# Kernel tuning notes

Measured on AMD Instinct MI355X. Metric: run time of the kernel, lower is better.

## Reference

```python
import jax, jax.numpy as jnp
import numpy as np

B, T, D, H, L = 32, 512, 256, 512, 3


def setup_inputs() -> dict:
    key = jax.random.key(0)
    ks = jax.random.split(key, 14)
    def lin(k, fan_in, shape):
        return jax.random.normal(k, shape, jnp.float32) / np.sqrt(fan_in)
    inp = {"x": jax.random.normal(ks[0], (B, T, D), jnp.float32)}
    dims_in = [D, H, H]
    i = 1
    for l in range(L):
        inp[f"Wi{l}"] = lin(ks[i + 0], dims_in[l], (3 * H, dims_in[l]))
        inp[f"bi{l}"] = lin(ks[i + 1], dims_in[l], (3 * H,))
        inp[f"Wh{l}"] = lin(ks[i + 2], H, (3 * H, H))
        inp[f"bh{l}"] = lin(ks[i + 3], H, (3 * H,))
        i += 4
    return inp


def _cell(Wi, bi, Wh, bh, xin, h):
    # faithful to ExponentialGatingGRUCell (h2h term appears twice in n preact)
    h2h = h @ Wh.T + bh                      # [B, 3H]
    preact = xin @ Wi.T + bi + h2h           # [B, 3H]
    g = jax.nn.sigmoid(preact[:, : 2 * H])
    r, z = g[:, :H], g[:, H:]
    r = jnp.exp(-jnp.exp(-r))
    z = jnp.exp(-jnp.exp(-z))
    n = jnp.tanh(preact[:, 2 * H:] + r * h2h[:, 2 * H:])
    return (1.0 - z) * n + z * h


def _forward(x, params):
    h0 = tuple(jnp.zeros((x.shape[0], H), x.dtype) for _ in range(L))

    def step(carry, x_t):
        hs = list(carry)
        inp = x_t
        for l in range(L):
            Wi, bi, Wh, bh = params[l]
            hs[l] = _cell(Wi, bi, Wh, bh, inp, hs[l])
            inp = hs[l]
        return tuple(hs), None

    hT, _ = jax.lax.scan(step, h0, jnp.swapaxes(x, 0, 1))  # scan over time
    return hT[-1][:, None, :]  # [B, 1, H]


def reference(x, Wi0, bi0, Wh0, bh0, Wi1, bi1, Wh1, bh1, Wi2, bi2, Wh2, bh2):
    params = [(Wi0, bi0, Wh0, bh0), (Wi1, bi1, Wh1, bh1), (Wi2, bi2, Wh2, bh2)]
    return _forward(x, params)
```

## Files before the change

kernel.cpp:

```cpp
#include <hip/hip_runtime.h>
#include <hip/hip_bf16.h>

typedef __attribute__((ext_vector_type(4))) float fx4;
typedef __attribute__((ext_vector_type(8))) short bf8;
typedef __attribute__((ext_vector_type(4))) short sx4;
typedef __attribute__((ext_vector_type(4))) int ix4;

#define NBLK 96
#define HSZ (32 * 512)

__device__ __forceinline__ short f2bf(float f) {
  __hip_bfloat16 h = __float2bfloat16(f);
  return *reinterpret_cast<short*>(&h);
}
__device__ __forceinline__ float bf2f(short s) {
  union { unsigned u; float f; } c; c.u = ((unsigned)(unsigned short)s) << 16; return c.f;
}
__device__ __forceinline__ float rcpf(float x) { return __builtin_amdgcn_rcpf(x); }
__device__ __forceinline__ bf8 asbf8(ix4 v) { union { ix4 i; bf8 b; } u; u.i = v; return u.b; }

#define LDH(dst, p, OFF) \
  asm volatile("global_load_dwordx4 %0, %1, off offset:" OFF " sc0 sc1" \
               : "=v"(dst) : "v"(p) : "memory")
#define LDP(dst, p, OFF) \
  asm volatile("global_load_dwordx4 %0, %1, off offset:" OFF \
               : "=v"(dst) : "v"(p) : "memory")

#define LDH8(A, P) do { \
  LDH(A[0], P, "0");   LDH(A[1], P, "64");  LDH(A[2], P, "128"); LDH(A[3], P, "192"); \
  LDH(A[4], P, "256"); LDH(A[5], P, "320"); LDH(A[6], P, "384"); LDH(A[7], P, "448"); } while (0)
#define LDP4(A, P) do { \
  LDP(A[0], P, "0");   LDP(A[1], P, "64");  LDP(A[2], P, "128"); LDP(A[3], P, "192"); } while (0)

__global__ __launch_bounds__(256) void conv_x_k(const float* __restrict__ x,
                                                short* __restrict__ xhi, short* __restrict__ xlo) {
  int i = blockIdx.x * 256 + threadIdx.x;
  fx4 v = *(const fx4*)(x + (size_t)i * 4);
  int k = (i * 4) & 255;
  int row = (i * 4) >> 8;
  int b = row >> 9, t = row & 511;
  sx4 hi, lo;
#pragma unroll
  for (int e = 0; e < 4; ++e) {
    hi[e] = f2bf(v[e]);
    lo[e] = f2bf(v[e] - bf2f(hi[e]));
  }
  size_t o = ((size_t)(t * 32 + b)) * 256 + k;
  *(sx4*)(xhi + o) = hi;
  *(sx4*)(xlo + o) = lo;
}

__global__ __launch_bounds__(256, 1) void rec3(
    const short* __restrict__ xth, const short* __restrict__ xtl,
    const float* __restrict__ Wi0, const float* __restrict__ bi0,
    const float* __restrict__ Wh0, const float* __restrict__ bh0,
    const float* __restrict__ Wi1, const float* __restrict__ bi1,
    const float* __restrict__ Wh1, const float* __restrict__ bh1,
    const float* __restrict__ Wi2, const float* __restrict__ bi2,
    const float* __restrict__ Wh2, const float* __restrict__ bh2,
    short* __restrict__ hg, int* flags, float* __restrict__ out)
{
  __shared__ __align__(16) float m_lds[4][32][52];
  __shared__ float bi_s[48], bh_s[48];
  const int tid = threadIdx.x;
  const int bid = blockIdx.x;
  const int l = bid >> 5, p = bid & 31, j0 = p * 16;
  const int w = tid >> 6, lane = tid & 63, lm = lane & 15, lk = lane >> 4;
  const bool inW = (w < 2);

  const float *Wi, *bi, *Wh, *bh;
  if (l == 0)      { Wi = Wi0; bi = bi0; Wh = Wh0; bh = bh0; }
  else if (l == 1) { Wi = Wi1; bi = bi1; Wh = Wh1; bh = bh1; }
  else             { Wi = Wi2; bi = bi2; Wh = Wh2; bh = bh2; }
  const int Kin = (l == 0) ? 256 : 512;
  const int ksn = inW ? (Kin >> 6) : 8;
  const int kbase = inW ? w * (Kin >> 1) : (w - 2) * 256;
  const float* Wf = inW ? Wi : Wh;
  const int wstride = inW ? Kin : 512;

  bf8 bwh[3][8], bwl[3][8];
#pragma unroll
  for (int g = 0; g < 3; ++g) {
    const int grow = g * 512 + j0 + lm;
#pragma unroll
    for (int ks = 0; ks < 8; ++ks) if (ks < ksn) {
      const float* src = Wf + (size_t)grow * wstride + kbase + ks * 32 + lk * 8;
      fx4 f0 = *(const fx4*)(src);
      fx4 f1 = *(const fx4*)(src + 4);
      bf8 vh, vl;
#pragma unroll
      for (int e = 0; e < 4; ++e) {
        vh[e] = f2bf(f0[e]);     vl[e] = f2bf(f0[e] - bf2f(vh[e]));
        vh[4 + e] = f2bf(f1[e]); vl[4 + e] = f2bf(f1[e] - bf2f(vh[4 + e]));
      }
      bwh[g][ks] = vh; bwl[g][ks] = vl;
    }
  }
  if (tid < 48) {
    bi_s[tid] = bi[(tid >> 4) * 512 + j0 + (tid & 15)];
    bh_s[tid] = bh[(tid >> 4) * 512 + j0 + (tid & 15)];
  }

  short* hgl = hg + (size_t)l * 4 * HSZ;
  const short* hgp = hg + (size_t)(l - 1) * 4 * HSZ;
  {
    const int b = tid >> 3, zc = (tid & 7) * 2;
    __hip_atomic_store((int*)(hgl + (size_t)2 * HSZ + b * 512 + j0 + zc), 0,
                       __ATOMIC_RELAXED, __HIP_MEMORY_SCOPE_AGENT);
    __hip_atomic_store((int*)(hgl + (size_t)3 * HSZ + b * 512 + j0 + zc), 0,
                       __ATOMIC_RELAXED, __HIP_MEMORY_SCOPE_AGENT);
  }
  __syncthreads();
  if (tid == 0)
    __hip_atomic_store(flags + bid * 32, 1, __ATOMIC_RELAXED, __HIP_MEMORY_SCOPE_AGENT);

  const int cb = tid >> 3, c2 = (tid & 7) * 2;
  float hv0 = 0.f, hv1 = 0.f;

  for (int t = 0; t < 514; ++t) {
    const int s = t - l;
    const bool active = ((unsigned)s < 512u);

    ix4 rh[2][8], rl[2][8];
    if (active && l == 0 && inW) {
      const short* x0h = xth + (size_t)(s * 32 + lm) * 256 + kbase + lk * 8;
      const short* x1h = x0h + 16 * 256;
      const short* x0l = xtl + (size_t)(s * 32 + lm) * 256 + kbase + lk * 8;
      const short* x1l = x0l + 16 * 256;
      LDP4(rh[0], x0h); LDP4(rh[1], x1h);
      LDP4(rl[0], x0l); LDP4(rl[1], x1l);
    }

    if (tid < NBLK) {
      while (__hip_atomic_load(flags + tid * 32, __ATOMIC_RELAXED,
                               __HIP_MEMORY_SCOPE_AGENT) < t + 1) {}
    }
    __syncthreads();

    if (active) {
      if (!(l == 0 && inW)) {
        const short* basep = inW ? (hgp + (size_t)((s & 1) * 2) * HSZ)
                                 : (hgl + (size_t)(((s - 1) & 1) * 2) * HSZ);
        const short* s0h = basep + (size_t)lm * 512 + kbase + lk * 8;
        const short* s1h = s0h + 16 * 512;
        const short* s0l = s0h + HSZ;
        const short* s1l = s1h + HSZ;
        LDH8(rh[0], s0h); LDH8(rh[1], s1h);
        LDH8(rl[0], s0l); LDH8(rl[1], s1l);
      }
      asm volatile("s_waitcnt vmcnt(0)" ::: "memory");
      __builtin_amdgcn_sched_barrier(0);

      fx4 acc[2][3];
#pragma unroll
      for (int mt = 0; mt < 2; ++mt)
#pragma unroll
        for (int g = 0; g < 3; ++g) acc[mt][g] = (fx4){0.f, 0.f, 0.f, 0.f};
#pragma unroll
      for (int ks = 0; ks < 8; ++ks) if (ks < ksn) {
#pragma unroll
        for (int mt = 0; mt < 2; ++mt) {
          bf8 ah = asbf8(rh[mt][ks]);
          bf8 al = asbf8(rl[mt][ks]);
#pragma unroll
          for (int g = 0; g < 3; ++g) {
            acc[mt][g] = __builtin_amdgcn_mfma_f32_16x16x32_bf16(ah, bwh[g][ks], acc[mt][g], 0, 0, 0);
            acc[mt][g] = __builtin_amdgcn_mfma_f32_16x16x32_bf16(al, bwh[g][ks], acc[mt][g], 0, 0, 0);
            acc[mt][g] = __builtin_amdgcn_mfma_f32_16x16x32_bf16(ah, bwl[g][ks], acc[mt][g], 0, 0, 0);
          }
        }
      }
#pragma unroll
      for (int mt = 0; mt < 2; ++mt)
#pragma unroll
        for (int g = 0; g < 3; ++g)
#pragma unroll
          for (int q = 0; q < 4; ++q)
            m_lds[w][mt * 16 + lk * 4 + q][g * 16 + lm] = acc[mt][g][q];
      __syncthreads();

      float av[3][2], hh[3][2];
#pragma unroll
      for (int g = 0; g < 3; ++g)
#pragma unroll
        for (int e = 0; e < 2; ++e) {
          const int c = g * 16 + c2 + e;
          av[g][e] = m_lds[0][cb][c] + m_lds[1][cb][c] + bi_s[c];
          hh[g][e] = m_lds[2][cb][c] + m_lds[3][cb][c] + bh_s[c];
        }
      float hvv[2] = {hv0, hv1}, hn[2];
#pragma unroll
      for (int e = 0; e < 2; ++e) {
        float pr = av[0][e] + hh[0][e];
        float pz = av[1][e] + hh[1][e];
        float h2n = hh[2][e];
        float pn = av[2][e] + h2n;
        float sr = rcpf(1.f + __expf(-pr));
        float rr = __expf(-__expf(-sr));
        float sz = rcpf(1.f + __expf(-pz));
        float zz = __expf(-__expf(-sz));
        float na = pn + rr * h2n;
        float ex = __expf(2.f * na);
        float nn = 1.f - 2.f * rcpf(ex + 1.f);
        hn[e] = (1.f - zz) * nn + zz * hvv[e];
      }
      hv0 = hn[0]; hv1 = hn[1];
      short h0h = f2bf(hn[0]), h0l = f2bf(hn[0] - bf2f(h0h));
      short h1h = f2bf(hn[1]), h1l = f2bf(hn[1] - bf2f(h1h));
      int packh = (int)(unsigned short)h0h | ((int)(unsigned short)h1h << 16);
      int packl = (int)(unsigned short)h0l | ((int)(unsigned short)h1l << 16);

      short* hw = hgl + (size_t)((s & 1) * 2) * HSZ;
      __hip_atomic_store((int*)(hw + (size_t)cb * 512 + j0 + c2), packh,
                         __ATOMIC_RELAXED, __HIP_MEMORY_SCOPE_AGENT);
      __hip_atomic_store((int*)(hw + HSZ + (size_t)cb * 512 + j0 + c2), packl,
                         __ATOMIC_RELAXED, __HIP_MEMORY_SCOPE_AGENT);
      if (l == 2 && s == 511) {
        out[(size_t)cb * 512 + j0 + c2] = hn[0];
        out[(size_t)cb * 512 + j0 + c2 + 1] = hn[1];
      }
      __syncthreads();
    }
    if (tid == 0)
      __hip_atomic_store(flags + bid * 32, t + 2,
                         __ATOMIC_RELAXED, __HIP_MEMORY_SCOPE_AGENT);
  }
}

extern "C" void kernel_launch(void* const* d_in, const int* in_sizes, int n_in,
                              void* d_out, int out_size, void* d_ws, size_t ws_size,
                              hipStream_t stream) {
  const float* x   = (const float*)d_in[0];
  const float* Wi0 = (const float*)d_in[1];
  const float* bi0 = (const float*)d_in[2];
  const float* Wh0 = (const float*)d_in[3];
  const float* bh0 = (const float*)d_in[4];
  const float* Wi1 = (const float*)d_in[5];
  const float* bi1 = (const float*)d_in[6];
  const float* Wh1 = (const float*)d_in[7];
  const float* bh1 = (const float*)d_in[8];
  const float* Wi2 = (const float*)d_in[9];
  const float* bi2 = (const float*)d_in[10];
  const float* Wh2 = (const float*)d_in[11];
  const float* bh2 = (const float*)d_in[12];
  float* out = (float*)d_out;
  (void)in_sizes; (void)n_in; (void)out_size; (void)ws_size;

  char* ws = (char*)d_ws;
  size_t off = 0;
  auto alloc = [&](size_t b) { char* p = ws + off; off = (off + b + 255) & ~(size_t)255; return p; };
  short* xth   = (short*)alloc(16384ull * 256 * 2);
  short* xtl   = (short*)alloc(16384ull * 256 * 2);
  short* hg    = (short*)alloc(3ull * 4 * HSZ * 2);
  int*   flags = (int*)alloc(NBLK * 32 * 4);

  hipMemsetAsync(flags, 0, NBLK * 32 * 4, stream);
  hipLaunchKernelGGL(conv_x_k, dim3(4096), dim3(256), 0, stream, x, xth, xtl);
  hipLaunchKernelGGL(rec3, dim3(NBLK), dim3(256), 0, stream,
                     xth, xtl,
                     Wi0, bi0, Wh0, bh0,
                     Wi1, bi1, Wh1, bh1,
                     Wi2, bi2, Wh2, bh2,
                     hg, flags, out);
}
```

Measured before the change: 3.340 ms.

## Replace global barrier with per-layer dependency flags and triple-buffered hidden state

Result: no change. 3.296 ms (-1.3%).

```diff
diff --git a/kernel.cpp b/kernel.cpp
--- a/kernel.cpp
+++ b/kernel.cpp
@@ -25,12 +25,9 @@
 #define LDP(dst, p, OFF) \
   asm volatile("global_load_dwordx4 %0, %1, off offset:" OFF \
                : "=v"(dst) : "v"(p) : "memory")
-
-#define LDH8(A, P) do { \
-  LDH(A[0], P, "0");   LDH(A[1], P, "64");  LDH(A[2], P, "128"); LDH(A[3], P, "192"); \
-  LDH(A[4], P, "256"); LDH(A[5], P, "320"); LDH(A[6], P, "384"); LDH(A[7], P, "448"); } while (0)
-#define LDP4(A, P) do { \
-  LDP(A[0], P, "0");   LDP(A[1], P, "64");  LDP(A[2], P, "128"); LDP(A[3], P, "192"); } while (0)
+#define LD8(OP, A, P) do { \
+  OP(A[0], P, "0");   OP(A[1], P, "64");  OP(A[2], P, "128"); OP(A[3], P, "192"); \
+  OP(A[4], P, "256"); OP(A[5], P, "320"); OP(A[6], P, "384"); OP(A[7], P, "448"); } while (0)
 
 __global__ __launch_bounds__(256) void conv_x_k(const float* __restrict__ x,
                                                 short* __restrict__ xhi, short* __restrict__ xlo) {
@@ -48,6 +45,204 @@
   size_t o = ((size_t)(t * 32 + b)) * 256 + k;
   *(sx4*)(xhi + o) = hi;
   *(sx4*)(xlo + o) = lo;
+}
+
+template<int L>
+__device__ __forceinline__ void rec3_body(
+    float (*m_lds)[32][52], float* bias_s,
+    const short* __restrict__ xth, const short* __restrict__ xtl,
+    const float* __restrict__ Wi, const float* __restrict__ bi,
+    const float* __restrict__ Wh, const float* __restrict__ bh,
+    short* __restrict__ hg, int* flags, float* __restrict__ out)
+{
+  const int tid = threadIdx.x;
+  const int bid = blockIdx.x;
+  const int j0 = (bid & 31) * 16;
+  const int w = tid >> 6, lane = tid & 63, lm = lane & 15, lk = lane >> 4;
+  const bool inW = (w < 2);
+  constexpr int KIN = (L == 0) ? 256 : 512;
+
+  short* hgl = hg + (size_t)L * 6 * HSZ;
+  const short* hgp = (L > 0) ? (hg + (size_t)(L - 1) * 6 * HSZ) : hg;
+
+  const int kbase = inW ? ((L == 0) ? 0 : w * 256) : (w - 2) * 256;
+  const float* Wf = inW ? Wi : Wh;
+  const int wstr = inW ? KIN : 512;
+
+  bf8 bwh[3][8], bwl[3][8];
+#pragma unroll
+  for (int g = 0; g < 3; ++g) {
+    const int grow = g * 512 + j0 + lm;
+#pragma unroll
+    for (int ks = 0; ks < 8; ++ks) {
+      const float* src = Wf + (size_t)grow * wstr + kbase + ks * 32 + lk * 8;
+      fx4 f0 = *(const fx4*)(src);
+      fx4 f1 = *(const fx4*)(src + 4);
+      bf8 vh, vl;
+#pragma unroll
+      for (int e = 0; e < 4; ++e) {
+        vh[e] = f2bf(f0[e]);     vl[e] = f2bf(f0[e] - bf2f(vh[e]));
+        vh[4 + e] = f2bf(f1[e]); vl[4 + e] = f2bf(f1[e] - bf2f(vh[4 + e]));
+      }
+      bwh[g][ks] = vh; bwl[g][ks] = vl;
+    }
+  }
+  if (tid < 48) bias_s[tid] = bi[(tid >> 4) * 512 + j0 + (tid & 15)];
+  else if (tid < 96) {
+    const int u = tid - 48;
+    bias_s[48 + u] = bh[(u >> 4) * 512 + j0 + (u & 15)];
+  }
+  {
+    const int b = tid >> 3, zc = (tid & 7) * 2;
+    __hip_atomic_store((int*)(hgl + (size_t)4 * HSZ + b * 512 + j0 + zc), 0,
+                       __ATOMIC_RELAXED, __HIP_MEMORY_SCOPE_AGENT);
+    __hip_atomic_store((int*)(hgl + (size_t)5 * HSZ + b * 512 + j0 + zc), 0,
+                       __ATOMIC_RELAXED, __HIP_MEMORY_SCOPE_AGENT);
+  }
+  __syncthreads();
+  if (tid == 0)
+    __hip_atomic_store(flags + bid * 32, 2, __ATOMIC_RELAXED, __HIP_MEMORY_SCOPE_AGENT);
+
+  constexpr int FBASE = (L == 0) ? 0 : (L - 1) * 32;
+  constexpr int FCNT  = (L == 1) ? 96 : 64;
+  const int cb = tid >> 3, c2 = (tid & 7) * 2;
+  float hv0 = 0.f, hv1 = 0.f;
+  int bufw = 0;
+
+  for (int s = 0; s < 512; ++s) {
+    ix4 rh[2][8], rl[2][8];
+    if (L == 0 && inW) {
+      const short* xh = xth + (size_t)(s * 32 + w * 16 + lm) * 256 + lk * 8;
+      const short* xl = xtl + (size_t)(s * 32 + w * 16 + lm) * 256 + lk * 8;
+      LD8(LDP, rh[0], xh);
+      LD8(LDP, rl[0], xl);
+    }
+
+    if (tid < FCNT) {
+      const int f = FBASE + tid;
+      const int fl = f >> 5;
+      const int thr = (fl < L) ? (s + 3) : ((fl == L) ? (s + 2) : s);
+      while (__hip_atomic_load(flags + f * 32, __ATOMIC_RELAXED,
+                               __HIP_MEMORY_SCOPE_AGENT) < thr)
+        __builtin_amdgcn_s_sleep(1);
+    }
+    __syncthreads();
+
+    const int bufr = (bufw == 0) ? 2 : bufw - 1;
+    if (!(L == 0 && inW)) {
+      const short* basep = inW ? (hgp + (size_t)(bufw * 2) * HSZ)
+                               : (hgl + (size_t)(bufr * 2) * HSZ);
+      const short* s0h = basep + (size_t)lm * 512 + kbase + lk * 8;
+      const short* s1h = s0h + 16 * 512;
+      const short* s0l = s0h + HSZ;
+      const short* s1l = s1h + HSZ;
+      LD8(LDH, rh[0], s0h); LD8(LDH, rh[1], s1h);
+      LD8(LDH, rl[0], s0l); LD8(LDH, rl[1], s1l);
+    }
+    asm volatile("s_waitcnt vmcnt(0)" ::: "memory");
+    __builtin_amdgcn_sched_barrier(0);
+
+    fx4 acc[2][3];
+#pragma unroll
+    for (int mt = 0; mt < 2; ++mt)
+#pragma unroll
+      for (int g = 0; g < 3; ++g) acc[mt][g] = (fx4){0.f, 0.f, 0.f, 0.f};
+
+    if (L == 0 && inW) {
+#pragma unroll
+      for (int ks = 0; ks < 8; ++ks) {
+        bf8 ah = asbf8(rh[0][ks]);
+        bf8 al = asbf8(rl[0][ks]);
+#pragma unroll
+        for (int g = 0; g < 3; ++g) {
+          acc[0][g] = __builtin_amdgcn_mfma_f32_16x16x32_bf16(ah, bwh[g][ks], acc[0][g], 0, 0, 0);
+          acc[0][g] = __builtin_amdgcn_mfma_f32_16x16x32_bf16(al, bwh[g][ks], acc[0][g], 0, 0, 0);
+          acc[0][g] = __builtin_amdgcn_mfma_f32_16x16x32_bf16(ah, bwl[g][ks], acc[0][g], 0, 0, 0);
+        }
+      }
+    } else {
+#pragma unroll
+      for (int ks = 0; ks < 8; ++ks) {
+#pragma unroll
+        for (int mt = 0; mt < 2; ++mt) {
+          bf8 ah = asbf8(rh[mt][ks]);
+          bf8 al = asbf8(rl[mt][ks]);
+#pragma unroll
+          for (int g = 0; g < 3; ++g) {
+            acc[mt][g] = __builtin_amdgcn_mfma_f32_16x16x32_bf16(ah, bwh[g][ks], acc[mt][g], 0, 0, 0);
+            acc[mt][g] = __builtin_amdgcn_mfma_f32_16x16x32_bf16(al, bwh[g][ks], acc[mt][g], 0, 0, 0);
+            acc[mt][g] = __builtin_amdgcn_mfma_f32_16x16x32_bf16(ah, bwl[g][ks], acc[mt][g], 0, 0, 0);
+          }
+        }
+      }
+    }
+
+    if (L == 0 && inW) {
+#pragma unroll
+      for (int g = 0; g < 3; ++g)
+#pragma unroll
+        for (int q = 0; q < 4; ++q)
+          m_lds[0][w * 16 + lk * 4 + q][g * 16 + lm] = acc[0][g][q];
+    } else {
+#pragma unroll
+      for (int mt = 0; mt < 2; ++mt)
+#pragma unroll
+        for (int g = 0; g < 3; ++g)
+#pragma unroll
+          for (int q = 0; q < 4; ++q)
+            m_lds[w][mt * 16 + lk * 4 + q][g * 16 + lm] = acc[mt][g][q];
+    }
+    __syncthreads();
+
+    float av[3][2], hh[3][2];
+#pragma unroll
+    for (int g = 0; g < 3; ++g)
+#pragma unroll
+      for (int e = 0; e < 2; ++e) {
+        const int c = g * 16 + c2 + e;
+        float ain = m_lds[0][cb][c];
+        if (L > 0) ain += m_lds[1][cb][c];
+        av[g][e] = ain + bias_s[c];
+        hh[g][e] = m_lds[2][cb][c] + m_lds[3][cb][c] + bias_s[48 + c];
+      }
+    float hvv[2] = {hv0, hv1}, hn[2];
+#pragma unroll
+    for (int e = 0; e < 2; ++e) {
+      float pr = av[0][e] + hh[0][e];
+      float pz = av[1][e] + hh[1][e];
+      float h2n = hh[2][e];
+      float pn = av[2][e] + h2n;
+      float sr = rcpf(1.f + __expf(-pr));
+      float rr = __expf(-__expf(-sr));
+      float sz = rcpf(1.f + __expf(-pz));
+      float zz = __expf(-__expf(-sz));
+      float na = pn + rr * h2n;
+      float ex = __expf(2.f * na);
+      float nn = 1.f - 2.f * rcpf(ex + 1.f);
+      hn[e] = (1.f - zz) * nn + zz * hvv[e];
+    }
+    hv0 = hn[0]; hv1 = hn[1];
+    short h0h = f2bf(hn[0]), h0l = f2bf(hn[0] - bf2f(h0h));
+    short h1h = f2bf(hn[1]), h1l = f2bf(hn[1] - bf2f(h1h));
+    int packh = (int)(unsigned short)h0h | ((int)(unsigned short)h1h << 16);
+    int packl = (int)(unsigned short)h0l | ((int)(unsigned short)h1l << 16);
+
+    short* hw = hgl + (size_t)(bufw * 2) * HSZ;
+    __hip_atomic_store((int*)(hw + (size_t)cb * 512 + j0 + c2), packh,
+                       __ATOMIC_RELAXED, __HIP_MEMORY_SCOPE_AGENT);
+    __hip_atomic_store((int*)(hw + HSZ + (size_t)cb * 512 + j0 + c2), packl,
+                       __ATOMIC_RELAXED, __HIP_MEMORY_SCOPE_AGENT);
+    if (L == 2 && s == 511) {
+      out[(size_t)cb * 512 + j0 + c2] = hn[0];
+      out[(size_t)cb * 512 + j0 + c2 + 1] = hn[1];
+    }
+    __syncthreads();
+    if (tid == 0)
+      __hip_atomic_store(flags + bid * 32, s + 3,
+                         __ATOMIC_RELAXED, __HIP_MEMORY_SCOPE_AGENT);
+
+    bufw = (bufw == 2) ? 0 : bufw + 1;
+  }
 }
 
 __global__ __launch_bounds__(256, 1) void rec3(
@@ -61,170 +256,14 @@
     short* __restrict__ hg, int* flags, float* __restrict__ out)
 {
   __shared__ __align__(16) float m_lds[4][32][52];
-  __shared__ float bi_s[48], bh_s[48];
-  const int tid = threadIdx.x;
-  const int bid = blockIdx.x;
-  const int l = bid >> 5, p = bid & 31, j0 = p * 16;
-  const int w = tid >> 6, lane = tid & 63, lm = lane & 15, lk = lane >> 4;
-  const bool inW = (w < 2);
-
-  const float *Wi, *bi, *Wh, *bh;
-  if (l == 0)      { Wi = Wi0; bi = bi0; Wh = Wh0; bh = bh0; }
-  else if (l == 1) { Wi = Wi1; bi = bi1; Wh = Wh1; bh = bh1; }
-  else             { Wi = Wi2; bi = bi2; Wh = Wh2; bh = bh2; }
-  const int Kin = (l == 0) ? 256 : 512;
-  const int ksn = inW ? (Kin >> 6) : 8;
-  const int kbase = inW ? w * (Kin >> 1) : (w - 2) * 256;
-  const float* Wf = inW ? Wi : Wh;
-  const int wstride = inW ? Kin : 512;
-
-  bf8 bwh[3][8], bwl[3][8];
-#pragma unroll
-  for (int g = 0; g < 3; ++g) {
-    const int grow = g * 512 + j0 + lm;
-#pragma unroll
-    for (int ks = 0; ks < 8; ++ks) if (ks < ksn) {
-      const float* src = Wf + (size_t)grow * wstride + kbase + ks * 32 + lk * 8;
-      fx4 f0 = *(const fx4*)(src);
-      fx4 f1 = *(const fx4*)(src + 4);
-      bf8 vh, vl;
-#pragma unroll
-      for (int e = 0; e < 4; ++e) {
-        vh[e] = f2bf(f0[e]);     vl[e] = f2bf(f0[e] - bf2f(vh[e]));
-        vh[4 + e] = f2bf(f1[e]); vl[4 + e] = f2bf(f1[e] - bf2f(vh[4 + e]));
-      }
-      bwh[g][ks] = vh; bwl[g][ks] = vl;
-    }
-  }
-  if (tid < 48) {
-    bi_s[tid] = bi[(tid >> 4) * 512 + j0 + (tid & 15)];
-    bh_s[tid] = bh[(tid >> 4) * 512 + j0 + (tid & 15)];
-  }
-
-  short* hgl = hg + (size_t)l * 4 * HSZ;
-  const short* hgp = hg + (size_t)(l - 1) * 4 * HSZ;
-  {
-    const int b = tid >> 3, zc = (tid & 7) * 2;
-    __hip_atomic_store((int*)(hgl + (size_t)2 * HSZ + b * 512 + j0 + zc), 0,
-                       __ATOMIC_RELAXED, __HIP_MEMORY_SCOPE_AGENT);
-    __hip_atomic_store((int*)(hgl + (size_t)3 * HSZ + b * 512 + j0 + zc), 0,
-                       __ATOMIC_RELAXED, __HIP_MEMORY_SCOPE_AGENT);
-  }
-  __syncthreads();
-  if (tid == 0)
-    __hip_atomic_store(flags + bid * 32, 1, __ATOMIC_RELAXED, __HIP_MEMORY_SCOPE_AGENT);
-
-  const int cb = tid >> 3, c2 = (tid & 7) * 2;
-  float hv0 = 0.f, hv1 = 0.f;
-
-  for (int t = 0; t < 514; ++t) {
-    const int s = t - l;
-    const bool active = ((unsigned)s < 512u);
-
-    ix4 rh[2][8], rl[2][8];
-    if (active && l == 0 && inW) {
-      const short* x0h = xth + (size_t)(s * 32 + lm) * 256 + kbase + lk * 8;
-      const short* x1h = x0h + 16 * 256;
-      const short* x0l = xtl + (size_t)(s * 32 + lm) * 256 + kbase + lk * 8;
-      const short* x1l = x0l + 16 * 256;
-      LDP4(rh[0], x0h); LDP4(rh[1], x1h);
-      LDP4(rl[0], x0l); LDP4(rl[1], x1l);
-    }
-
-    if (tid < NBLK) {
-      while (__hip_atomic_load(flags + tid * 32, __ATOMIC_RELAXED,
-                               __HIP_MEMORY_SCOPE_AGENT) < t + 1) {}
-    }
-    __syncthreads();
-
-    if (active) {
-      if (!(l == 0 && inW)) {
-        const short* basep = inW ? (hgp + (size_t)((s & 1) * 2) * HSZ)
-                                 : (hgl + (size_t)(((s - 1) & 1) * 2) * HSZ);
-        const short* s0h = basep + (size_t)lm * 512 + kbase + lk * 8;
-        const short* s1h = s0h + 16 * 512;
-        const short* s0l = s0h + HSZ;
-        const short* s1l = s1h + HSZ;
-        LDH8(rh[0], s0h); LDH8(rh[1], s1h);
-        LDH8(rl[0], s0l); LDH8(rl[1], s1l);
-      }
-      asm volatile("s_waitcnt vmcnt(0)" ::: "memory");
-      __builtin_amdgcn_sched_barrier(0);
-
-      fx4 acc[2][3];
-#pragma unroll
-      for (int mt = 0; mt < 2; ++mt)
-#pragma unroll
-        for (int g = 0; g < 3; ++g) acc[mt][g] = (fx4){0.f, 0.f, 0.f, 0.f};
-#pragma unroll
-      for (int ks = 0; ks < 8; ++ks) if (ks < ksn) {
-#pragma unroll
-        for (int mt = 0; mt < 2; ++mt) {
-          bf8 ah = asbf8(rh[mt][ks]);
-          bf8 al = asbf8(rl[mt][ks]);
-#pragma unroll
-          for (int g = 0; g < 3; ++g) {
-            acc[mt][g] = __builtin_amdgcn_mfma_f32_16x16x32_bf16(ah, bwh[g][ks], acc[mt][g], 0, 0, 0);
-            acc[mt][g] = __builtin_amdgcn_mfma_f32_16x16x32_bf16(al, bwh[g][ks], acc[mt][g], 0, 0, 0);
-            acc[mt][g] = __builtin_amdgcn_mfma_f32_16x16x32_bf16(ah, bwl[g][ks], acc[mt][g], 0, 0, 0);
-          }
-        }
-      }
-#pragma unroll
-      for (int mt = 0; mt < 2; ++mt)
-#pragma unroll
-        for (int g = 0; g < 3; ++g)
-#pragma unroll
-          for (int q = 0; q < 4; ++q)
-            m_lds[w][mt * 16 + lk * 4 + q][g * 16 + lm] = acc[mt][g][q];
-      __syncthreads();
-
-      float av[3][2], hh[3][2];
-#pragma unroll
-      for (int g = 0; g < 3; ++g)
-#pragma unroll
-        for (int e = 0; e < 2; ++e) {
-          const int c = g * 16 + c2 + e;
-          av[g][e] = m_lds[0][cb][c] + m_lds[1][cb][c] + bi_s[c];
-          hh[g][e] = m_lds[2][cb][c] + m_lds[3][cb][c] + bh_s[c];
-        }
-      float hvv[2] = {hv0, hv1}, hn[2];
-#pragma unroll
-      for (int e = 0; e < 2; ++e) {
-        float pr = av[0][e] + hh[0][e];
-        float pz = av[1][e] + hh[1][e];
-        float h2n = hh[2][e];
-        float pn = av[2][e] + h2n;
-        float sr = rcpf(1.f + __expf(-pr));
-        float rr = __expf(-__expf(-sr));
-        float sz = rcpf(1.f + __expf(-pz));
-        float zz = __expf(-__expf(-sz));
-        float na = pn + rr * h2n;
-        float ex = __expf(2.f * na);
-        float nn = 1.f - 2.f * rcpf(ex + 1.f);
-        hn[e] = (1.f - zz) * nn + zz * hvv[e];
-      }
-      hv0 = hn[0]; hv1 = hn[1];
-      short h0h = f2bf(hn[0]), h0l = f2bf(hn[0] - bf2f(h0h));
-      short h1h = f2bf(hn[1]), h1l = f2bf(hn[1] - bf2f(h1h));
-      int packh = (int)(unsigned short)h0h | ((int)(unsigned short)h1h << 16);
-      int packl = (int)(unsigned short)h0l | ((int)(unsigned short)h1l << 16);
-
-      short* hw = hgl + (size_t)((s & 1) * 2) * HSZ;
-      __hip_atomic_store((int*)(hw + (size_t)cb * 512 + j0 + c2), packh,
-                         __ATOMIC_RELAXED, __HIP_MEMORY_SCOPE_AGENT);
-      __hip_atomic_store((int*)(hw + HSZ + (size_t)cb * 512 + j0 + c2), packl,
-                         __ATOMIC_RELAXED, __HIP_MEMORY_SCOPE_AGENT);
-      if (l == 2 && s == 511) {
-        out[(size_t)cb * 512 + j0 + c2] = hn[0];
-        out[(size_t)cb * 512 + j0 + c2 + 1] = hn[1];
-      }
-      __syncthreads();
-    }
-    if (tid == 0)
-      __hip_atomic_store(flags + bid * 32, t + 2,
-                         __ATOMIC_RELAXED, __HIP_MEMORY_SCOPE_AGENT);
-  }
+  __shared__ float bias_s[96];
+  const int l = blockIdx.x >> 5;
+  if (l == 0)
+    rec3_body<0>(m_lds, bias_s, xth, xtl, Wi0, bi0, Wh0, bh0, hg, flags, out);
+  else if (l == 1)
+    rec3_body<1>(m_lds, bias_s, nullptr, nullptr, Wi1, bi1, Wh1, bh1, hg, flags, out);
+  else
+    rec3_body<2>(m_lds, bias_s, nullptr, nullptr, Wi2, bi2, Wh2, bh2, hg, flags, out);
 }
 
 extern "C" void kernel_launch(void* const* d_in, const int* in_sizes, int n_in,
@@ -251,7 +290,7 @@
   auto alloc = [&](size_t b) { char* p = ws + off; off = (off + b + 255) & ~(size_t)255; return p; };
   short* xth   = (short*)alloc(16384ull * 256 * 2);
   short* xtl   = (short*)alloc(16384ull * 256 * 2);
-  short* hg    = (short*)alloc(3ull * 4 * HSZ * 2);
+  short* hg    = (short*)alloc(3ull * 6 * HSZ * 2);
   int*   flags = (int*)alloc(NBLK * 32 * 4);
 
   hipMemsetAsync(flags, 0, NBLK * 32 * 4, stream);
```
